# Kernel tuning notes

Measured on AMD Instinct MI355X. Metric: run time of the kernel, lower is better.

The kernel has to match this reference:

```python
import jax, jax.numpy as jnp
import numpy as np

L = 2        # n_layer
D = 1024     # hidden_size
H = 8        # n_head
DK = D // H  # head_dim = 128
DV = D // H
T = 2048     # max_seq_length
B = 4
INTER = 2816 # fla GatedMLP: int(1024*4*2/3)=2730 rounded up to multiple of 256
EPS = 1e-6


def rmsnorm(x, w):
    return x * jax.lax.rsqrt(jnp.mean(x * x, axis=-1, keepdims=True) + EPS) * w


def l2norm(x):
    return x * jax.lax.rsqrt(jnp.sum(x * x, axis=-1, keepdims=True) + EPS)


def delta_attn(x, Wq, Wk, Wv, Wb, Wo, onorm_w):
    # x: [B, T, D]
    b, t, _ = x.shape
    q = jax.nn.silu((x @ Wq).reshape(b, t, H, DK))
    k = jax.nn.silu((x @ Wk).reshape(b, t, H, DK))
    q = l2norm(q)
    k = l2norm(k)
    v = jax.nn.silu((x @ Wv).reshape(b, t, H, DV))
    beta = jax.nn.sigmoid(x @ Wb) * 2.0  # [B,T,H], allow_neg_eigval=True
    # time-major for scan
    qt = q.transpose(1, 0, 2, 3)  # [T,B,H,DK]
    kt = k.transpose(1, 0, 2, 3)
    vt = v.transpose(1, 0, 2, 3)
    bt = beta.transpose(1, 0, 2)  # [T,B,H]

    def step(S, inps):
        qi, ki, vi, bi = inps
        # delta rule: S_t = S_{t-1} + beta_t * k_t (v_t - S_{t-1}^T k_t)^T
        pred = jnp.einsum('bhkv,bhk->bhv', S, ki)
        S = S + bi[..., None, None] * ki[..., :, None] * (vi - pred)[..., None, :]
        o = jnp.einsum('bhkv,bhk->bhv', S, qi)
        return S, o

    S0 = jnp.zeros((b, H, DK, DV), x.dtype)
    _, o = jax.lax.scan(step, S0, (qt, kt, vt, bt))  # o: [T,B,H,DV]
    o = rmsnorm(o, onorm_w)  # per-head RMSNorm (use_gate=False)
    o = o.transpose(1, 0, 2, 3).reshape(b, t, H * DV)
    return o @ Wo


def setup_inputs() -> dict:
    key = jax.random.key(0)
    ks = jax.random.split(key, 13)
    s = 0.02
    f32 = jnp.float32
    return {
        'input_embeds': jax.random.normal(ks[0], (T, B, D), f32),
        'Wq': jax.random.normal(ks[1], (L, D, D), f32) * s,
        'Wk': jax.random.normal(ks[2], (L, D, D), f32) * s,
        'Wv': jax.random.normal(ks[3], (L, D, D), f32) * s,
        'Wb': jax.random.normal(ks[4], (L, D, H), f32) * s,
        'Wo': jax.random.normal(ks[5], (L, D, D), f32) * s,
        'onorm_w': jnp.ones((L, DV), f32) + jax.random.normal(ks[6], (L, DV), f32) * 0.02,
        'norm1_w': jnp.ones((L, D), f32) + jax.random.normal(ks[7], (L, D), f32) * 0.02,
        'norm2_w': jnp.ones((L, D), f32) + jax.random.normal(ks[8], (L, D), f32) * 0.02,
        'Wg': jax.random.normal(ks[9], (L, D, 2 * INTER), f32) * s,
        'Wd': jax.random.normal(ks[10], (L, INTER, D), f32) * s,
        'final_norm_w': jnp.ones((D,), f32) + jax.random.normal(ks[11], (D,), f32) * 0.02,
    }


def reference(input_embeds, Wq, Wk, Wv, Wb, Wo, onorm_w, norm1_w, norm2_w, Wg, Wd, final_norm_w):
    # wrapper transposes (T,B,D) -> (B,T,D)
    x = input_embeds.transpose(1, 0, 2)
    for l in range(L):
        h = rmsnorm(x, norm1_w[l])
        x = x + delta_attn(h, Wq[l], Wk[l], Wv[l], Wb[l], Wo[l], onorm_w[l])
        h = rmsnorm(x, norm2_w[l])
        gy = h @ Wg[l]
        g, y = jnp.split(gy, 2, axis=-1)
        x = x + (jax.nn.silu(g) * y) @ Wd[l]
    x = rmsnorm(x, final_norm_w)
    return x.transpose(1, 0, 2)  # back to (T,B,D)
```

## Files before the change

kernel.cpp:

```cpp
#include <hip/hip_runtime.h>
#include <hip/hip_bf16.h>
#include <cstdint>


typedef _Float16 f16;
typedef __attribute__((ext_vector_type(8))) _Float16 h8;
typedef __attribute__((ext_vector_type(4))) _Float16 h4;
typedef __attribute__((ext_vector_type(4))) float f4;

#define DEV __device__ __forceinline__

static constexpr int Bb_ = 4;
static constexpr int Hh  = 8;
static constexpr int Dd  = 1024;
static constexpr int Tt  = 2048;
static constexpr int NC  = 32;

DEV float siluf(float x) { return x / (1.f + expf(-x)); }

#define AS1(p) ((const __attribute__((address_space(1))) void*)(uintptr_t)(p))
#define AS3(p) ((__attribute__((address_space(3))) void*)(uint32_t)(uintptr_t)(p))

DEV void stage_half(const f16* __restrict__ srcRowBase, int K, int kt,
                    f16* dstHalf, int tid) {
#pragma unroll
  for (int i = 0; i < 2; ++i) {
    const int q = i * 512 + tid;
    const int r = q >> 3, cs = q & 7;
    const int cl = cs ^ (r & 7);
    __builtin_amdgcn_global_load_lds(AS1(srcRowBase + (size_t)r * K + kt * 64 + cl * 8),
                                     AS3(dstHalf + q * 8), 16, 0, 0);
  }
}
DEV h8 rd_sw(const f16* T, int row, int chunk) {
  return *(const h8*)(T + (((row << 3) | (chunk ^ (row & 7))) * 8));
}

template<int EPI, int BN>
__global__ __launch_bounds__(512, 2) void gemm2(const f16* __restrict__ A, const f16* __restrict__ Bt,
                                                void* __restrict__ C, const f16* __restrict__ Yp,
                                                int M, int N, int K, int gx) {
  constexpr int NCF = BN / 64;
  __shared__ __align__(16) f16 ldsA[2][16384];
  __shared__ __align__(16) f16 ldsB[2][BN * 64];
  const int tid = threadIdx.x, lane = tid & 63, w = tid >> 6;
  const int l15 = lane & 15, l4 = lane >> 4;
  const int wr = w >> 2, wc = w & 3;
  const int nwg = gridDim.x;
  int flat = blockIdx.x;
  if ((nwg & 7) == 0) flat = (flat & 7) * (nwg >> 3) + (flat >> 3);
  const int bx = flat % gx, by = flat / gx;

  const f16* Ab = A + (size_t)by * 256 * K;
  const f16* Bb = Bt + (size_t)bx * BN * K;
  const int NT = K >> 6;
  f4 acc[8][NCF] = {};

  stage_half(Bb, K, 0, ldsB[0], tid);
  if (BN == 256) stage_half(Bb + (size_t)128 * K, K, 0, ldsB[0] + 8192, tid);
  stage_half(Ab, K, 0, ldsA[0], tid);
  stage_half(Ab + (size_t)128 * K, K, 0, ldsA[0] + 8192, tid);
  if (NT > 1) {
    stage_half(Bb, K, 1, ldsB[1], tid);
    if (BN == 256) stage_half(Bb + (size_t)128 * K, K, 1, ldsB[1] + 8192, tid);
    if (BN == 256) asm volatile("s_waitcnt vmcnt(4)");
    else           asm volatile("s_waitcnt vmcnt(2)");
  } else {
    asm volatile("s_waitcnt vmcnt(0)");
  }
  __builtin_amdgcn_s_barrier();

  for (int t = 0; t < NT; ++t) {
    const int cur = t & 1, nxt = cur ^ 1;
    const f16* cA = ldsA[cur];
    const f16* cB = ldsB[cur];
    h8 b[NCF][2];
    h8 a[2][2];
#pragma unroll
    for (int cf = 0; cf < NCF; ++cf)
#pragma unroll
      for (int ks = 0; ks < 2; ++ks)
        b[cf][ks] = rd_sw(cB, wc * (BN / 4) + cf * 16 + l15, ks * 4 + l4);
#pragma unroll
    for (int fr = 0; fr < 2; ++fr)
#pragma unroll
      for (int ks = 0; ks < 2; ++ks)
        a[fr][ks] = rd_sw(cA, wr * 128 + fr * 16 + l15, ks * 4 + l4);
    if (t + 1 < NT) stage_half(Ab, K, t + 1, ldsA[nxt], tid);
    __builtin_amdgcn_s_barrier();
    asm volatile("s_waitcnt lgkmcnt(0)");
    __builtin_amdgcn_s_setprio(1);
#pragma unroll
    for (int fr = 0; fr < 2; ++fr)
#pragma unroll
      for (int cf = 0; cf < NCF; ++cf)
#pragma unroll
        for (int ks = 0; ks < 2; ++ks)
          acc[fr][cf] = __builtin_amdgcn_mfma_f32_16x16x32_f16(a[fr][ks], b[cf][ks], acc[fr][cf], 0, 0, 0);
    __builtin_amdgcn_s_setprio(0);
    __builtin_amdgcn_s_barrier();
#pragma unroll
    for (int p = 1; p < 4; ++p) {
#pragma unroll
      for (int fr = 0; fr < 2; ++fr)
#pragma unroll
        for (int ks = 0; ks < 2; ++ks)
          a[fr][ks] = rd_sw(cA, wr * 128 + p * 32 + fr * 16 + l15, ks * 4 + l4);
      if (p == 1 && t + 1 < NT) stage_half(Ab + (size_t)128 * K, K, t + 1, ldsA[nxt] + 8192, tid);
      if (p == 2 && t + 2 < NT) stage_half(Bb, K, t + 2, ldsB[cur], tid);
      if (BN == 256 && p == 3 && t + 2 < NT) stage_half(Bb + (size_t)128 * K, K, t + 2, ldsB[cur] + 8192, tid);
      __builtin_amdgcn_s_barrier();
      asm volatile("s_waitcnt lgkmcnt(0)");
      __builtin_amdgcn_s_setprio(1);
#pragma unroll
      for (int fr = 0; fr < 2; ++fr)
#pragma unroll
        for (int cf = 0; cf < NCF; ++cf)
#pragma unroll
          for (int ks = 0; ks < 2; ++ks)
            acc[p * 2 + fr][cf] = __builtin_amdgcn_mfma_f32_16x16x32_f16(a[fr][ks], b[cf][ks], acc[p * 2 + fr][cf], 0, 0, 0);
      __builtin_amdgcn_s_setprio(0);
      if (p == 3) {
        if (t + 2 < NT) {
          if (BN == 256) asm volatile("s_waitcnt vmcnt(4)");
          else           asm volatile("s_waitcnt vmcnt(2)");
        } else if (t + 1 < NT) {
          asm volatile("s_waitcnt vmcnt(0)");
        }
      }
      __builtin_amdgcn_s_barrier();
    }
  }

#pragma unroll
  for (int fr = 0; fr < 8; ++fr) {
#pragma unroll
    for (int cf = 0; cf < NCF; ++cf) {
      const int row0 = by * 256 + wr * 128 + fr * 16 + l4 * 4;
      const int col = bx * BN + wc * (BN / 4) + cf * 16 + l15;
#pragma unroll
      for (int q = 0; q < 4; ++q) {
        const size_t idx = (size_t)(row0 + q) * N + col;
        const float v = acc[fr][cf][q];
        if (EPI == 0) ((float*)C)[idx] = v;
        if (EPI == 1) ((f16*)C)[idx] = (f16)((float)((f16*)C)[idx] + v);
        if (EPI == 2) ((f16*)C)[idx] = (f16)v;
        if (EPI == 3) ((f16*)C)[idx] = (f16)(siluf(v) * (float)Yp[idx]);
      }
    }
  }
}

__global__ __launch_bounds__(256) void cvt_k(const float* __restrict__ in, f16* __restrict__ out) {
  const size_t i = ((size_t)blockIdx.x * 256 + threadIdx.x) * 8;
  const float4 a = *(const float4*)(in + i);
  const float4 b = *(const float4*)(in + i + 4);
  h8 o = {(f16)a.x, (f16)a.y, (f16)a.z, (f16)a.w, (f16)b.x, (f16)b.y, (f16)b.z, (f16)b.w};
  *(h8*)(out + i) = o;
}

template<int OUT_F16>
__global__ __launch_bounds__(256) void rmsnorm_k(const f16* __restrict__ x, const float* __restrict__ w,
                                                 void* __restrict__ out) {
  const int r = blockIdx.x, tid = threadIdx.x;
  const h4 xv = *(const h4*)(x + (size_t)r * 1024 + tid * 4);
  const float v0 = (float)xv[0], v1 = (float)xv[1], v2 = (float)xv[2], v3 = (float)xv[3];
  float ss = v0 * v0 + v1 * v1 + v2 * v2 + v3 * v3;
#pragma unroll
  for (int m = 1; m < 64; m <<= 1) ss += __shfl_xor(ss, m);
  __shared__ float red[4];
  if ((tid & 63) == 0) red[tid >> 6] = ss;
  __syncthreads();
  const float scale = rsqrtf((red[0] + red[1] + red[2] + red[3]) * (1.f / 1024.f) + 1e-6f);
  const float4 w4 = *(const float4*)(w + tid * 4);
  float o0 = v0 * scale * w4.x, o1 = v1 * scale * w4.y, o2 = v2 * scale * w4.z, o3 = v3 * scale * w4.w;
  if (OUT_F16) {
    h4 o = {(f16)o0, (f16)o1, (f16)o2, (f16)o3};
    *(h4*)((f16*)out + (size_t)r * 1024 + tid * 4) = o;
  } else {
    *(float4*)((float*)out + (size_t)r * 1024 + tid * 4) = make_float4(o0, o1, o2, o3);
  }
}

__global__ __launch_bounds__(256) void qkv_epi(const f16* __restrict__ qkv, f16* __restrict__ qb,
                                               f16* __restrict__ kb, f16* __restrict__ vb) {
  const int r = blockIdx.x, tid = threadIdx.x;
  const int head = tid >> 5, l32 = tid & 31;
  const size_t src = (size_t)r * 3072 + head * 128 + l32 * 4;
  const size_t dst = (size_t)r * 1024 + head * 128 + l32 * 4;
  {
    const h4 v = *(const h4*)(qkv + src);
    float s0 = siluf((float)v[0]), s1 = siluf((float)v[1]), s2 = siluf((float)v[2]), s3 = siluf((float)v[3]);
    float ss = s0 * s0 + s1 * s1 + s2 * s2 + s3 * s3;
#pragma unroll
    for (int m = 1; m <= 16; m <<= 1) ss += __shfl_xor(ss, m);
    const float sc = rsqrtf(ss + 1e-6f);
    h4 o = {(f16)(s0 * sc), (f16)(s1 * sc), (f16)(s2 * sc), (f16)(s3 * sc)};
    *(h4*)(qb + dst) = o;
  }
  {
    const h4 v = *(const h4*)(qkv + src + 1024);
    float s0 = siluf((float)v[0]), s1 = siluf((float)v[1]), s2 = siluf((float)v[2]), s3 = siluf((float)v[3]);
    float ss = s0 * s0 + s1 * s1 + s2 * s2 + s3 * s3;
#pragma unroll
    for (int m = 1; m <= 16; m <<= 1) ss += __shfl_xor(ss, m);
    const float sc = rsqrtf(ss + 1e-6f);
    h4 o = {(f16)(s0 * sc), (f16)(s1 * sc), (f16)(s2 * sc), (f16)(s3 * sc)};
    *(h4*)(kb + dst) = o;
  }
  {
    const h4 v = *(const h4*)(qkv + (size_t)r * 3072 + 2048 + tid * 4);
    h4 o = {(f16)siluf((float)v[0]), (f16)siluf((float)v[1]), (f16)siluf((float)v[2]), (f16)siluf((float)v[3])};
    *(h4*)(vb + (size_t)r * 1024 + tid * 4) = o;
  }
}

__global__ __launch_bounds__(256) void onorm_k(const float* __restrict__ o, const float* __restrict__ w,
                                               f16* __restrict__ ob) {
  const int r = blockIdx.x, tid = threadIdx.x;
  const int head = tid >> 5, l32 = tid & 31;
  const size_t base = (size_t)r * 1024 + head * 128 + l32 * 4;
  const float4 v = *(const float4*)(o + base);
  float ss = v.x * v.x + v.y * v.y + v.z * v.z + v.w * v.w;
#pragma unroll
  for (int m = 1; m <= 16; m <<= 1) ss += __shfl_xor(ss, m);
  const float sc = rsqrtf(ss * (1.f / 128.f) + 1e-6f);
  const float4 w4 = *(const float4*)(w + l32 * 4);
  h4 out = {(f16)(v.x * sc * w4.x), (f16)(v.y * sc * w4.y), (f16)(v.z * sc * w4.z), (f16)(v.w * sc * w4.w)};
  *(h4*)(ob + base) = out;
}

__global__ __launch_bounds__(256) void beta_k(const f16* __restrict__ hb, const float* __restrict__ Wb,
                                              float* __restrict__ beta) {
  const int tid = threadIdx.x, lane = tid & 63, wv = tid >> 6;
  const int r = blockIdx.x * 4 + wv;
  const f16* row = hb + (size_t)r * 1024 + lane * 16;
  const h8 v0 = *(const h8*)(row);
  const h8 v1 = *(const h8*)(row + 8);
  const float* wb = Wb + (size_t)(lane * 16) * 8;
  float acc[8] = {};
#pragma unroll
  for (int e = 0; e < 8; ++e) {
    const float x0 = (float)v0[e], x1 = (float)v1[e];
    const float4 w0a = *(const float4*)(wb + e * 8);
    const float4 w0b = *(const float4*)(wb + e * 8 + 4);
    const float4 w1a = *(const float4*)(wb + (e + 8) * 8);
    const float4 w1b = *(const float4*)(wb + (e + 8) * 8 + 4);
    acc[0] += x0 * w0a.x + x1 * w1a.x;  acc[1] += x0 * w0a.y + x1 * w1a.y;
    acc[2] += x0 * w0a.z + x1 * w1a.z;  acc[3] += x0 * w0a.w + x1 * w1a.w;
    acc[4] += x0 * w0b.x + x1 * w1b.x;  acc[5] += x0 * w0b.y + x1 * w1b.y;
    acc[6] += x0 * w0b.z + x1 * w1b.z;  acc[7] += x0 * w0b.w + x1 * w1b.w;
  }
#pragma unroll
  for (int j = 0; j < 8; ++j)
#pragma unroll
    for (int m = 1; m < 64; m <<= 1) acc[j] += __shfl_xor(acc[j], m);
  if (lane == 0) {
#pragma unroll
    for (int j = 0; j < 8; ++j) beta[(size_t)r * 8 + j] = 2.f / (1.f + expf(-acc[j]));
  }
}

__global__ __launch_bounds__(256) void transpose_k(const float* __restrict__ W, f16* __restrict__ Wt,
                                                   int K, int N) {
  __shared__ float tile[32][33];
  const int n0 = blockIdx.x * 32, k0 = blockIdx.y * 32;
  const int tx = threadIdx.x & 31, ty = threadIdx.x >> 5;
#pragma unroll
  for (int i = 0; i < 32; i += 8) tile[ty + i][tx] = W[(size_t)(k0 + ty + i) * N + n0 + tx];
  __syncthreads();
#pragma unroll
  for (int i = 0; i < 32; i += 8) Wt[(size_t)(n0 + ty + i) * K + k0 + tx] = (f16)tile[tx][ty + i];
}

__global__ void fill_k(float* p, int n, float v) {
  const int i = blockIdx.x * 256 + threadIdx.x;
  if (i < n) p[i] = v;
}

DEV f4 mm16(const f16* A, int as, const f16* B, f4 c, int l15, int l4) {
  h4 a = *(const h4*)(A + l15 * as + l4 * 4);
  h4 b = *(const h4*)(B + l15 * 20 + l4 * 4);
  return __builtin_amdgcn_mfma_f32_16x16x16f16(a, b, c, 0, 0, 0);
}
DEV void wr_T(f16* slot, f4 acc, int l15, int l4, float sgn) {
  h4 v = {(f16)(sgn * acc[0]), (f16)(sgn * acc[1]), (f16)(sgn * acc[2]), (f16)(sgn * acc[3])};
  *(h4*)(slot + l15 * 20 + l4 * 4) = v;
}
DEV void wr_Tb(f16* Tb, int bi, int bj, f4 acc, const float* betas, int l15, int l4, float sgn) {
  const float bc = betas[bj * 16 + l15];
#pragma unroll
  for (int q = 0; q < 4; ++q)
    Tb[(bi * 16 + l4 * 4 + q) * 72 + bj * 16 + l15] = (f16)(sgn * acc[q] * bc);
}

__global__ __launch_bounds__(256) void phaseA(const f16* __restrict__ kb, const f16* __restrict__ qb,
                                              const f16* __restrict__ vb, const float* __restrict__ beta,
                                              f16* __restrict__ wbuf, f16* __restrict__ ubuf,
                                              f16* __restrict__ pbuf) {
  const int blk = blockIdx.x;
  const int c = blk >> 5, bh = blk & 31;
  const int b = bh >> 3, h = bh & 7;
  const int tid = threadIdx.x, lane = tid & 63, wv = tid >> 6;
  const int l15 = lane & 15, l4 = lane >> 4;

  __shared__ __align__(16) f16 Ks[64 * 128];
  __shared__ __align__(16) f16 QVs[64 * 128];
  __shared__ __align__(16) f16 Abuf[64 * 68];
  __shared__ __align__(16) f16 Dr[4][16 * 20];
  __shared__ __align__(16) f16 Dt[4][16 * 20];
  __shared__ __align__(16) f16 Tp[3][16 * 20];
  __shared__ __align__(16) f16 Xp[3][16 * 20];
  __shared__ __align__(16) f16 Tb[64 * 72];
  __shared__ float betas[64];

  const size_t rowstr = (size_t)Bb_ * Dd;
  const size_t gbase = ((size_t)(c * 64) * Bb_ + b) * Dd + h * 128;

#pragma unroll
  for (int i = 0; i < 4; ++i) {
    const int ch = tid + i * 256;
    const int rr = ch >> 4, kc = ch & 15;
    *(h8*)(Ks + ch * 8) = *(const h8*)(kb + gbase + (size_t)rr * rowstr + kc * 8);
    *(h8*)(QVs + ch * 8) = *(const h8*)(qb + gbase + (size_t)rr * rowstr + kc * 8);
  }
  for (int i = tid; i < 64 * 72; i += 256) Tb[i] = (f16)0.f;
  if (tid < 64) betas[tid] = beta[((size_t)(c * 64 + tid) * Bb_ + b) * Hh + h];
  __syncthreads();

  f4 accS[4] = {}, accP[4] = {};
  const int arow = wv * 16 + l15;
  const int koff = l4 * 8;
#pragma unroll
  for (int kc = 0; kc < 4; ++kc) {
    const h8 aK = *(const h8*)(Ks + arow * 128 + kc * 32 + koff);
    const h8 aQ = *(const h8*)(QVs + arow * 128 + kc * 32 + koff);
#pragma unroll
    for (int f = 0; f < 4; ++f) {
      const h8 bK = *(const h8*)(Ks + (f * 16 + l15) * 128 + kc * 32 + koff);
      accS[f] = __builtin_amdgcn_mfma_f32_16x16x32_f16(aK, bK, accS[f], 0, 0, 0);
      accP[f] = __builtin_amdgcn_mfma_f32_16x16x32_f16(aQ, bK, accP[f], 0, 0, 0);
    }
  }
  const size_t pbase = (((size_t)bh * NC + c) * 64) * 64;
#pragma unroll
  for (int f = 0; f < 4; ++f) {
#pragma unroll
    for (int q = 0; q < 4; ++q) {
      const int i = wv * 16 + l4 * 4 + q;
      const int j = f * 16 + l15;
      Abuf[i * 68 + j] = (f16)((j < i) ? betas[i] * accS[f][q] : 0.f);
      pbuf[pbase + (size_t)i * 64 + j] = (f16)((j <= i) ? accP[f][q] : 0.f);
    }
  }
  __syncthreads();

#pragma unroll
  for (int i = 0; i < 4; ++i) {
    const int ch = tid + i * 256;
    const int rr = ch >> 4, kc = ch & 15;
    *(h8*)(QVs + ch * 8) = *(const h8*)(vb + gbase + (size_t)rr * rowstr + kc * 8);
  }

  {
    const int bi = wv;
    const int cc = l15;
    const f16* Ad = Abuf + (bi * 16) * 68 + bi * 16;
    float t[16];
    t[0] = (cc == 0) ? 1.f : 0.f;
#pragma unroll
    for (int i = 1; i < 16; ++i) {
      float s = (cc == i) ? 1.f : 0.f;
#pragma unroll
      for (int j = 0; j < i; ++j) s -= (float)Ad[i * 68 + j] * t[j];
      t[i] = s;
    }
    if (lane < 16) {
#pragma unroll
      for (int j4 = 0; j4 < 4; ++j4) {
        h4 v = {(f16)t[j4 * 4], (f16)t[j4 * 4 + 1], (f16)t[j4 * 4 + 2], (f16)t[j4 * 4 + 3]};
        *(h4*)(&Dt[bi][cc * 20 + j4 * 4]) = v;
      }
      const float bc = betas[bi * 16 + cc];
#pragma unroll
      for (int j = 0; j < 16; ++j) {
        Dr[bi][j * 20 + cc] = (f16)t[j];
        Tb[(bi * 16 + j) * 72 + bi * 16 + cc] = (f16)(t[j] * bc);
      }
    }
  }
  __syncthreads();

  const f16* AB10 = Abuf + 16 * 68 + 0;
  const f16* AB20 = Abuf + 32 * 68 + 0;
  const f16* AB21 = Abuf + 32 * 68 + 16;
  const f16* AB30 = Abuf + 48 * 68 + 0;
  const f16* AB31 = Abuf + 48 * 68 + 16;
  const f16* AB32 = Abuf + 48 * 68 + 32;
  f4 z = {};
  f4 x20, x30;

  if (wv == 0) wr_T(Xp[0], mm16(AB10, 68, Dt[0], z, l15, l4), l15, l4, 1.f);
  if (wv == 1) wr_T(Xp[1], mm16(AB21, 68, Dt[1], z, l15, l4), l15, l4, 1.f);
  if (wv == 2) wr_T(Xp[2], mm16(AB32, 68, Dt[2], z, l15, l4), l15, l4, 1.f);
  if (wv == 3) x20 = mm16(AB20, 68, Dt[0], z, l15, l4);
  __syncthreads();
  if (wv == 0) { f4 r = mm16(Dr[1], 20, Xp[0], z, l15, l4); wr_T(Tp[0], r, l15, l4, -1.f); wr_Tb(Tb, 1, 0, r, betas, l15, l4, -1.f); }
  if (wv == 1) { f4 r = mm16(Dr[2], 20, Xp[1], z, l15, l4); wr_T(Tp[1], r, l15, l4, -1.f); wr_Tb(Tb, 2, 1, r, betas, l15, l4, -1.f); }
  if (wv == 2) { f4 r = mm16(Dr[3], 20, Xp[2], z, l15, l4); wr_Tb(Tb, 3, 2, r, betas, l15, l4, -1.f); }
  if (wv == 3) x30 = mm16(AB30, 68, Dt[0], z, l15, l4);
  __syncthreads();
  if (wv == 3) wr_T(Xp[0], mm16(AB21, 68, Tp[0], x20, l15, l4), l15, l4, 1.f);
  if (wv == 1) { f4 r = mm16(AB31, 68, Dt[1], z, l15, l4); r = mm16(AB32, 68, Tp[1], r, l15, l4); wr_T(Xp[1], r, l15, l4, 1.f); }
  __syncthreads();
  if (wv == 3) { f4 r = mm16(Dr[2], 20, Xp[0], z, l15, l4); wr_T(Tp[2], r, l15, l4, -1.f); wr_Tb(Tb, 2, 0, r, betas, l15, l4, -1.f); }
  if (wv == 1) { f4 r = mm16(Dr[3], 20, Xp[1], z, l15, l4); wr_Tb(Tb, 3, 1, r, betas, l15, l4, -1.f); }
  __syncthreads();
  if (wv == 3) { f4 r = mm16(AB31, 68, Tp[0], x30, l15, l4); r = mm16(AB32, 68, Tp[2], r, l15, l4); wr_T(Xp[2], r, l15, l4, 1.f); }
  __syncthreads();
  if (wv == 3) { f4 r = mm16(Dr[3], 20, Xp[2], z, l15, l4); wr_Tb(Tb, 3, 0, r, betas, l15, l4, -1.f); }
  __syncthreads();

  const size_t wub = ((size_t)bh * Tt + c * 64) * 128;
  f4 wacc[8] = {}, uacc[8] = {};
#pragma unroll
  for (int kc = 0; kc < 2; ++kc) {
    const h8 aT = *(const h8*)(Tb + (wv * 16 + l15) * 72 + kc * 32 + koff);
#pragma unroll
    for (int f = 0; f < 8; ++f) {
      h8 bK, bV;
#pragma unroll
      for (int j = 0; j < 8; ++j) {
        const int t2 = kc * 32 + koff + j;
        const int d = f * 16 + l15;
        bK[j] = Ks[t2 * 128 + d];
        bV[j] = QVs[t2 * 128 + d];
      }
      wacc[f] = __builtin_amdgcn_mfma_f32_16x16x32_f16(aT, bK, wacc[f], 0, 0, 0);
      uacc[f] = __builtin_amdgcn_mfma_f32_16x16x32_f16(aT, bV, uacc[f], 0, 0, 0);
    }
  }
#pragma unroll
  for (int f = 0; f < 8; ++f)
#pragma unroll
    for (int q = 0; q < 4; ++q) {
      const int i = wv * 16 + l4 * 4 + q;
      const int d = f * 16 + l15;
      wbuf[wub + (size_t)i * 128 + d] = (f16)wacc[f][q];
      ubuf[wub + (size_t)i * 128 + d] = (f16)uacc[f][q];
    }
}

__global__ __launch_bounds__(256) void phaseB(const f16* __restrict__ qb, const f16* __restrict__ kb,
                                              const f16* __restrict__ wbuf, const f16* __restrict__ ubuf,
                                              const f16* __restrict__ pbuf, float* __restrict__ obuf) {
  const int blk = blockIdx.x;
  const int bh = blk >> 2, g = blk & 3;
  const int b = bh >> 3, h = bh & 7;
  const int tid = threadIdx.x, lane = tid & 63, wv = tid >> 6;
  const int l15 = lane & 15, l4 = lane >> 4;

  __shared__ __align__(16) f16 Ws[64 * 128];
  __shared__ __align__(16) f16 Qs[64 * 128];
  __shared__ __align__(16) f16 Ks[64 * 128];
  __shared__ __align__(16) f16 Ps[64 * 64];
  __shared__ __align__(16) f16 Rt[32 * 72];
  __shared__ __align__(16) f16 Ms[32 * 136];

  for (int i = tid; i < 32 * 136; i += 256) Ms[i] = (f16)0.f;
  f4 macc[2][2] = {};

  const size_t rowstr = (size_t)Bb_ * Dd;
  const size_t qk0 = (size_t)b * Dd + h * 128;
  const int arow = wv * 16 + l15;
  const int koff = l4 * 8;
  __syncthreads();

  for (int c = 0; c < NC; ++c) {
    const size_t wub = ((size_t)bh * Tt + c * 64) * 128;
    const size_t pbase = (((size_t)bh * NC + c) * 64) * 64;
#pragma unroll
    for (int i = 0; i < 4; ++i) {
      const int ch = tid + i * 256;
      const int rr = ch >> 4, kc = ch & 15;
      *(h8*)(Ws + ch * 8) = *(const h8*)(wbuf + wub + ch * 8);
      *(h8*)(Qs + ch * 8) = *(const h8*)(qb + qk0 + (size_t)(c * 64 + rr) * rowstr + kc * 8);
      *(h8*)(Ks + ch * 8) = *(const h8*)(kb + qk0 + (size_t)(c * 64 + rr) * rowstr + kc * 8);
    }
#pragma unroll
    for (int i = 0; i < 2; ++i) {
      const int ch = tid + i * 256;
      *(h8*)(Ps + ch * 8) = *(const h8*)(pbuf + pbase + ch * 8);
    }
    __syncthreads();

    f4 accR[2] = {}, accO[2] = {};
#pragma unroll
    for (int kc = 0; kc < 4; ++kc) {
      const h8 aW = *(const h8*)(Ws + arow * 128 + kc * 32 + koff);
      const h8 aQ = *(const h8*)(Qs + arow * 128 + kc * 32 + koff);
#pragma unroll
      for (int f = 0; f < 2; ++f) {
        const h8 bM = *(const h8*)(Ms + (f * 16 + l15) * 136 + kc * 32 + koff);
        accR[f] = __builtin_amdgcn_mfma_f32_16x16x32_f16(aW, bM, accR[f], 0, 0, 0);
        accO[f] = __builtin_amdgcn_mfma_f32_16x16x32_f16(aQ, bM, accO[f], 0, 0, 0);
      }
    }
#pragma unroll
    for (int f = 0; f < 2; ++f) {
#pragma unroll
      for (int q = 0; q < 4; ++q) {
        const int i = wv * 16 + l4 * 4 + q;
        const int cc = f * 16 + l15;
        const float uv = (float)ubuf[wub + (size_t)i * 128 + g * 32 + cc];
        const float rv = uv - accR[f][q];
        accR[f][q] = rv;
        Rt[cc * 72 + i] = (f16)rv;
      }
    }
    __syncthreads();

#pragma unroll
    for (int kc = 0; kc < 2; ++kc) {
      const h8 aP = *(const h8*)(Ps + arow * 64 + kc * 32 + koff);
#pragma unroll
      for (int f = 0; f < 2; ++f) {
        const h8 bR = *(const h8*)(Rt + (f * 16 + l15) * 72 + kc * 32 + koff);
        accO[f] = __builtin_amdgcn_mfma_f32_16x16x32_f16(aP, bR, accO[f], 0, 0, 0);
      }
    }
#pragma unroll
    for (int f = 0; f < 2; ++f)
#pragma unroll
      for (int q = 0; q < 4; ++q) {
        const int i = wv * 16 + l4 * 4 + q;
        const int cc = f * 16 + l15;
        obuf[((size_t)(c * 64 + i) * Bb_ + b) * Dd + h * 128 + g * 32 + cc] = accO[f][q];
      }

#pragma unroll
    for (int kc = 0; kc < 2; ++kc) {
      const h8 aR0 = *(const h8*)(Rt + l15 * 72 + kc * 32 + koff);
      const h8 aR1 = *(const h8*)(Rt + (16 + l15) * 72 + kc * 32 + koff);
#pragma unroll
      for (int cf = 0; cf < 2; ++cf) {
        const int kcol = wv * 32 + cf * 16 + l15;
        h8 bKv;
#pragma unroll
        for (int j = 0; j < 8; ++j) bKv[j] = Ks[(kc * 32 + koff + j) * 128 + kcol];
        macc[0][cf] = __builtin_amdgcn_mfma_f32_16x16x32_f16(aR0, bKv, macc[0][cf], 0, 0, 0);
        macc[1][cf] = __builtin_amdgcn_mfma_f32_16x16x32_f16(aR1, bKv, macc[1][cf], 0, 0, 0);
      }
    }
#pragma unroll
    for (int rf = 0; rf < 2; ++rf)
#pragma unroll
      for (int cf = 0; cf < 2; ++cf)
#pragma unroll
        for (int q = 0; q < 4; ++q) {
          const int cr = rf * 16 + l4 * 4 + q;
          const int kcol = wv * 32 + cf * 16 + l15;
          Ms[cr * 136 + kcol] = (f16)macc[rf][cf][q];
        }
    __syncthreads();
  }
}

extern "C" void kernel_launch(void* const* d_in, const int* in_sizes, int n_in,
                              void* d_out, int out_size, void* d_ws, size_t ws_size,
                              hipStream_t stream) {
  (void)in_sizes; (void)n_in;
  const float* input = (const float*)d_in[0];
  const float* Wq = (const float*)d_in[1];
  const float* Wk = (const float*)d_in[2];
  const float* Wv = (const float*)d_in[3];
  const float* Wb = (const float*)d_in[4];
  const float* Wo = (const float*)d_in[5];
  const float* onw = (const float*)d_in[6];
  const float* n1w = (const float*)d_in[7];
  const float* n2w = (const float*)d_in[8];
  const float* Wg = (const float*)d_in[9];
  const float* Wd = (const float*)d_in[10];
  const float* fnw = (const float*)d_in[11];

  char* ws = (char*)d_ws;
  size_t off = 0;
  auto alloc = [&](size_t bytes) { void* p = ws + off; off += (bytes + 255) & ~(size_t)255; return p; };
  const size_t RD = 8192ull * 1024ull;
  f16*  x     = (f16*)alloc(RD * 2);
  f16*  hb    = (f16*)alloc(RD * 2);
  f16*  qb    = (f16*)alloc(RD * 2);
  f16*  kbuf  = (f16*)alloc(RD * 2);
  f16*  vbuf  = (f16*)alloc(RD * 2);
  float* beta = (float*)alloc(8192ull * 8 * 4);
  f16*  wbuf  = (f16*)alloc(RD * 2);
  f16*  ubuf  = (f16*)alloc(RD * 2);
  f16*  pbuf  = (f16*)alloc(32ull * 32 * 64 * 64 * 2);
  char* arena = (char*)alloc(3 * RD * 2);
  f16*  WqkvT = (f16*)alloc(3072ull * 1024 * 2);
  f16*  WoT   = (f16*)alloc(1024ull * 1024 * 2);
  f16*  WgT   = (f16*)alloc(5632ull * 1024 * 2);
  f16*  WdT   = (f16*)alloc(1024ull * 2816 * 2);
  if (off > ws_size) {
    fill_k<<<(out_size + 255) / 256, 256, 0, stream>>>((float*)d_out, out_size, 1.0e6f);
    return;
  }
  f16* qkvraw = (f16*)arena;
  float* obuf = (float*)arena;
  f16* Ybuf = (f16*)arena;
  f16* my = qb;
  f16* ob = wbuf;

  cvt_k<<<4096, 256, 0, stream>>>(input, x);

  for (int l = 0; l < 2; ++l) {
    const size_t o2 = (size_t)l * 1024 * 1024;
    transpose_k<<<dim3(32, 32), 256, 0, stream>>>(Wq + o2, WqkvT, 1024, 1024);
    transpose_k<<<dim3(32, 32), 256, 0, stream>>>(Wk + o2, WqkvT + 1024ull * 1024, 1024, 1024);
    transpose_k<<<dim3(32, 32), 256, 0, stream>>>(Wv + o2, WqkvT + 2048ull * 1024, 1024, 1024);
    transpose_k<<<dim3(32, 32), 256, 0, stream>>>(Wo + o2, WoT, 1024, 1024);
    transpose_k<<<dim3(176, 32), 256, 0, stream>>>(Wg + (size_t)l * 1024 * 5632, WgT, 1024, 5632);
    transpose_k<<<dim3(32, 88), 256, 0, stream>>>(Wd + (size_t)l * 2816 * 1024, WdT, 2816, 1024);

    rmsnorm_k<1><<<8192, 256, 0, stream>>>(x, n1w + l * 1024, hb);
    gemm2<2, 256><<<32 * 12, 512, 0, stream>>>(hb, WqkvT, qkvraw, nullptr, 8192, 3072, 1024, 12);
    beta_k<<<2048, 256, 0, stream>>>(hb, Wb + (size_t)l * 1024 * 8, beta);
    qkv_epi<<<8192, 256, 0, stream>>>(qkvraw, qb, kbuf, vbuf);
    phaseA<<<1024, 256, 0, stream>>>(kbuf, qb, vbuf, beta, wbuf, ubuf, pbuf);
    phaseB<<<128, 256, 0, stream>>>(qb, kbuf, wbuf, ubuf, pbuf, obuf);
    onorm_k<<<8192, 256, 0, stream>>>(obuf, onw + l * 128, ob);
    gemm2<1, 128><<<32 * 8, 512, 0, stream>>>(ob, WoT, x, nullptr, 8192, 1024, 1024, 8);

    rmsnorm_k<1><<<8192, 256, 0, stream>>>(x, n2w + l * 1024, hb);
    gemm2<2, 256><<<32 * 11, 512, 0, stream>>>(hb, WgT + 2816ull * 1024, Ybuf, nullptr, 8192, 2816, 1024, 11);
    gemm2<3, 256><<<32 * 11, 512, 0, stream>>>(hb, WgT, my, Ybuf, 8192, 2816, 1024, 11);
    gemm2<1, 128><<<32 * 8, 512, 0, stream>>>(my, WdT, x, nullptr, 8192, 1024, 2816, 8);
  }
  rmsnorm_k<0><<<8192, 256, 0, stream>>>(x, fnw, d_out);
}
```

Baseline: 1.142 ms.

## Double-buffer phaseB chunk loads, pre-transpose K/U, swizzle q/k/v layouts

New measurement: 1.064 ms. 6.8% less time.

```diff
diff --git a/kernel.cpp b/kernel.cpp
--- a/kernel.cpp
+++ b/kernel.cpp
@@ -17,6 +17,7 @@
 static constexpr int NC  = 32;
 
 DEV float siluf(float x) { return x / (1.f + expf(-x)); }
+DEV int swz16(int row, int c) { return (c & 8) | ((c & 7) ^ (row & 7)); }
 
 #define AS1(p) ((const __attribute__((address_space(1))) void*)(uintptr_t)(p))
 #define AS3(p) ((__attribute__((address_space(3))) void*)(uint32_t)(uintptr_t)(p))
@@ -186,8 +187,8 @@
                                                f16* __restrict__ kb, f16* __restrict__ vb) {
   const int r = blockIdx.x, tid = threadIdx.x;
   const int head = tid >> 5, l32 = tid & 31;
+  const int i = (r >> 2) & 63;
   const size_t src = (size_t)r * 3072 + head * 128 + l32 * 4;
-  const size_t dst = (size_t)r * 1024 + head * 128 + l32 * 4;
   {
     const h4 v = *(const h4*)(qkv + src);
     float s0 = siluf((float)v[0]), s1 = siluf((float)v[1]), s2 = siluf((float)v[2]), s3 = siluf((float)v[3]);
@@ -196,7 +197,8 @@
     for (int m = 1; m <= 16; m <<= 1) ss += __shfl_xor(ss, m);
     const float sc = rsqrtf(ss + 1e-6f);
     h4 o = {(f16)(s0 * sc), (f16)(s1 * sc), (f16)(s2 * sc), (f16)(s3 * sc)};
-    *(h4*)(qb + dst) = o;
+    const int c = l32 >> 1, off = (l32 & 1) * 4;
+    *(h4*)(qb + (size_t)r * 1024 + head * 128 + swz16(i, c) * 8 + off) = o;
   }
   {
     const h4 v = *(const h4*)(qkv + src + 1024);
@@ -206,27 +208,31 @@
     for (int m = 1; m <= 16; m <<= 1) ss += __shfl_xor(ss, m);
     const float sc = rsqrtf(ss + 1e-6f);
     h4 o = {(f16)(s0 * sc), (f16)(s1 * sc), (f16)(s2 * sc), (f16)(s3 * sc)};
-    *(h4*)(kb + dst) = o;
+    const int c = l32 >> 1, off = (l32 & 1) * 4;
+    *(h4*)(kb + (size_t)r * 1024 + head * 128 + swz16(i, c) * 8 + off) = o;
   }
   {
     const h4 v = *(const h4*)(qkv + (size_t)r * 3072 + 2048 + tid * 4);
     h4 o = {(f16)siluf((float)v[0]), (f16)siluf((float)v[1]), (f16)siluf((float)v[2]), (f16)siluf((float)v[3])};
-    *(h4*)(vb + (size_t)r * 1024 + tid * 4) = o;
-  }
-}
-
-__global__ __launch_bounds__(256) void onorm_k(const float* __restrict__ o, const float* __restrict__ w,
+    const int hd = tid >> 5, dh = (tid & 31) * 4;
+    const int c = dh >> 3, off = dh & 7;
+    *(h4*)(vb + (size_t)r * 1024 + hd * 128 + swz16(i, c) * 8 + off) = o;
+  }
+}
+
+__global__ __launch_bounds__(256) void onorm_k(const f16* __restrict__ o, const float* __restrict__ w,
                                                f16* __restrict__ ob) {
   const int r = blockIdx.x, tid = threadIdx.x;
   const int head = tid >> 5, l32 = tid & 31;
   const size_t base = (size_t)r * 1024 + head * 128 + l32 * 4;
-  const float4 v = *(const float4*)(o + base);
-  float ss = v.x * v.x + v.y * v.y + v.z * v.z + v.w * v.w;
+  const h4 xv = *(const h4*)(o + base);
+  const float v0 = (float)xv[0], v1 = (float)xv[1], v2 = (float)xv[2], v3 = (float)xv[3];
+  float ss = v0 * v0 + v1 * v1 + v2 * v2 + v3 * v3;
 #pragma unroll
   for (int m = 1; m <= 16; m <<= 1) ss += __shfl_xor(ss, m);
   const float sc = rsqrtf(ss * (1.f / 128.f) + 1e-6f);
   const float4 w4 = *(const float4*)(w + l32 * 4);
-  h4 out = {(f16)(v.x * sc * w4.x), (f16)(v.y * sc * w4.y), (f16)(v.z * sc * w4.z), (f16)(v.w * sc * w4.w)};
+  h4 out = {(f16)(v0 * sc * w4.x), (f16)(v1 * sc * w4.y), (f16)(v2 * sc * w4.z), (f16)(v3 * sc * w4.w)};
   *(h4*)(ob + base) = out;
 }
 
@@ -296,8 +302,8 @@
 
 __global__ __launch_bounds__(256) void phaseA(const f16* __restrict__ kb, const f16* __restrict__ qb,
                                               const f16* __restrict__ vb, const float* __restrict__ beta,
-                                              f16* __restrict__ wbuf, f16* __restrict__ ubuf,
-                                              f16* __restrict__ pbuf) {
+                                              f16* __restrict__ wbuf, f16* __restrict__ utbuf,
+                                              f16* __restrict__ pbuf, f16* __restrict__ ktbuf) {
   const int blk = blockIdx.x;
   const int c = blk >> 5, bh = blk & 31;
   const int b = bh >> 3, h = bh & 7;
@@ -330,14 +336,15 @@
 
   f4 accS[4] = {}, accP[4] = {};
   const int arow = wv * 16 + l15;
-  const int koff = l4 * 8;
 #pragma unroll
   for (int kc = 0; kc < 4; ++kc) {
-    const h8 aK = *(const h8*)(Ks + arow * 128 + kc * 32 + koff);
-    const h8 aQ = *(const h8*)(QVs + arow * 128 + kc * 32 + koff);
+    const int c4 = kc * 4 + l4;
+    const h8 aK = *(const h8*)(Ks + arow * 128 + swz16(arow, c4) * 8);
+    const h8 aQ = *(const h8*)(QVs + arow * 128 + swz16(arow, c4) * 8);
 #pragma unroll
     for (int f = 0; f < 4; ++f) {
-      const h8 bK = *(const h8*)(Ks + (f * 16 + l15) * 128 + kc * 32 + koff);
+      const int brow = f * 16 + l15;
+      const h8 bK = *(const h8*)(Ks + brow * 128 + swz16(brow, c4) * 8);
       accS[f] = __builtin_amdgcn_mfma_f32_16x16x32_f16(aK, bK, accS[f], 0, 0, 0);
       accP[f] = __builtin_amdgcn_mfma_f32_16x16x32_f16(aQ, bK, accP[f], 0, 0, 0);
     }
@@ -421,84 +428,111 @@
   if (wv == 3) { f4 r = mm16(Dr[3], 20, Xp[2], z, l15, l4); wr_Tb(Tb, 3, 0, r, betas, l15, l4, -1.f); }
   __syncthreads();
 
-  const size_t wub = ((size_t)bh * Tt + c * 64) * 128;
+  const size_t wub = ((size_t)bh * NC + c) * 8192;
+  const int koff = l4 * 8;
   f4 wacc[8] = {}, uacc[8] = {};
 #pragma unroll
   for (int kc = 0; kc < 2; ++kc) {
     const h8 aT = *(const h8*)(Tb + (wv * 16 + l15) * 72 + kc * 32 + koff);
 #pragma unroll
     for (int f = 0; f < 8; ++f) {
+      const int d = f * 16 + l15, cD = d >> 3, d7 = d & 7;
       h8 bK, bV;
 #pragma unroll
       for (int j = 0; j < 8; ++j) {
         const int t2 = kc * 32 + koff + j;
-        const int d = f * 16 + l15;
-        bK[j] = Ks[t2 * 128 + d];
-        bV[j] = QVs[t2 * 128 + d];
+        const int pos = t2 * 128 + swz16(t2, cD) * 8 + d7;
+        bK[j] = Ks[pos];
+        bV[j] = QVs[pos];
       }
       wacc[f] = __builtin_amdgcn_mfma_f32_16x16x32_f16(aT, bK, wacc[f], 0, 0, 0);
       uacc[f] = __builtin_amdgcn_mfma_f32_16x16x32_f16(aT, bV, uacc[f], 0, 0, 0);
     }
   }
 #pragma unroll
-  for (int f = 0; f < 8; ++f)
+  for (int f = 0; f < 8; ++f) {
+    const int d = f * 16 + l15, cD = d >> 3, d7 = d & 7;
 #pragma unroll
     for (int q = 0; q < 4; ++q) {
       const int i = wv * 16 + l4 * 4 + q;
-      const int d = f * 16 + l15;
-      wbuf[wub + (size_t)i * 128 + d] = (f16)wacc[f][q];
-      ubuf[wub + (size_t)i * 128 + d] = (f16)uacc[f][q];
-    }
-}
-
-__global__ __launch_bounds__(256) void phaseB(const f16* __restrict__ qb, const f16* __restrict__ kb,
-                                              const f16* __restrict__ wbuf, const f16* __restrict__ ubuf,
-                                              const f16* __restrict__ pbuf, float* __restrict__ obuf) {
+      wbuf[wub + (size_t)i * 128 + swz16(i, cD) * 8 + d7] = (f16)wacc[f][q];
+    }
+    h4 uv = {(f16)uacc[f][0], (f16)uacc[f][1], (f16)uacc[f][2], (f16)uacc[f][3]};
+    *(h4*)(utbuf + wub + (size_t)d * 64 + wv * 16 + l4 * 4) = uv;
+  }
+
+#pragma unroll
+  for (int i2 = 0; i2 < 4; ++i2) {
+    const int ch = tid + i2 * 256;
+    const int dp = ch & 127, c2 = ch >> 7;
+    h8 v;
+#pragma unroll
+    for (int j = 0; j < 8; ++j) {
+      const int i = c2 * 8 + j;
+      v[j] = Ks[i * 128 + swz16(i, dp >> 3) * 8 + (dp & 7)];
+    }
+    *(h8*)(ktbuf + wub + (size_t)dp * 64 + (c2 ^ (dp & 7)) * 8) = v;
+  }
+}
+
+__global__ __launch_bounds__(256) void phaseB(const f16* __restrict__ qb, const f16* __restrict__ ktbuf,
+                                              const f16* __restrict__ wbuf, const f16* __restrict__ utbuf,
+                                              const f16* __restrict__ pbuf, f16* __restrict__ obuf) {
   const int blk = blockIdx.x;
   const int bh = blk >> 2, g = blk & 3;
   const int b = bh >> 3, h = bh & 7;
   const int tid = threadIdx.x, lane = tid & 63, wv = tid >> 6;
   const int l15 = lane & 15, l4 = lane >> 4;
 
-  __shared__ __align__(16) f16 Ws[64 * 128];
-  __shared__ __align__(16) f16 Qs[64 * 128];
-  __shared__ __align__(16) f16 Ks[64 * 128];
-  __shared__ __align__(16) f16 Ps[64 * 64];
+  __shared__ __align__(16) f16 Ws[2][8192];
+  __shared__ __align__(16) f16 Qs[2][8192];
+  __shared__ __align__(16) f16 Kts[2][8192];
   __shared__ __align__(16) f16 Rt[32 * 72];
   __shared__ __align__(16) f16 Ms[32 * 136];
 
   for (int i = tid; i < 32 * 136; i += 256) Ms[i] = (f16)0.f;
   f4 macc[2][2] = {};
 
-  const size_t rowstr = (size_t)Bb_ * Dd;
-  const size_t qk0 = (size_t)b * Dd + h * 128;
   const int arow = wv * 16 + l15;
   const int koff = l4 * 8;
-  __syncthreads();
-
-  for (int c = 0; c < NC; ++c) {
-    const size_t wub = ((size_t)bh * Tt + c * 64) * 128;
-    const size_t pbase = (((size_t)bh * NC + c) * 64) * 64;
+
+  auto STAGE = [&](int c2, int buf) {
 #pragma unroll
     for (int i = 0; i < 4; ++i) {
       const int ch = tid + i * 256;
-      const int rr = ch >> 4, kc = ch & 15;
-      *(h8*)(Ws + ch * 8) = *(const h8*)(wbuf + wub + ch * 8);
-      *(h8*)(Qs + ch * 8) = *(const h8*)(qb + qk0 + (size_t)(c * 64 + rr) * rowstr + kc * 8);
-      *(h8*)(Ks + ch * 8) = *(const h8*)(kb + qk0 + (size_t)(c * 64 + rr) * rowstr + kc * 8);
-    }
-#pragma unroll
-    for (int i = 0; i < 2; ++i) {
-      const int ch = tid + i * 256;
-      *(h8*)(Ps + ch * 8) = *(const h8*)(pbuf + pbase + ch * 8);
-    }
-    __syncthreads();
+      const size_t tb = ((size_t)bh * NC + c2) * 8192;
+      __builtin_amdgcn_global_load_lds(AS1(wbuf + tb + ch * 8), AS3(Ws[buf] + ch * 8), 16, 0, 0);
+      __builtin_amdgcn_global_load_lds(AS1(ktbuf + tb + ch * 8), AS3(Kts[buf] + ch * 8), 16, 0, 0);
+      const int rr = ch >> 4, kc2 = ch & 15;
+      __builtin_amdgcn_global_load_lds(AS1(qb + ((size_t)((c2 * 64 + rr) * 4 + b)) * 1024 + h * 128 + kc2 * 8),
+                                       AS3(Qs[buf] + ch * 8), 16, 0, 0);
+    }
+  };
+
+  STAGE(0, 0);
+  asm volatile("s_waitcnt vmcnt(0)" ::: "memory");
+  __builtin_amdgcn_s_barrier();
+
+  for (int c = 0; c < NC; ++c) {
+    const int cur = c & 1, nxt = cur ^ 1;
+    const size_t pcb = ((size_t)bh * NC + c) * 4096;
+    const h8 aP0 = *(const h8*)(pbuf + pcb + arow * 64 + koff);
+    const h8 aP1 = *(const h8*)(pbuf + pcb + arow * 64 + 32 + koff);
+    const size_t ucb = ((size_t)bh * NC + c) * 8192;
+    const h4 u0 = *(const h4*)(utbuf + ucb + (size_t)(g * 32 + l15) * 64 + wv * 16 + l4 * 4);
+    const h4 u1 = *(const h4*)(utbuf + ucb + (size_t)(g * 32 + 16 + l15) * 64 + wv * 16 + l4 * 4);
+    asm volatile("s_waitcnt vmcnt(4)" ::: "memory");
+    asm volatile("s_waitcnt lgkmcnt(0)" ::: "memory");
+    __builtin_amdgcn_s_barrier();
+    if (c + 1 < NC) STAGE(c + 1, nxt);
 
     f4 accR[2] = {}, accO[2] = {};
+    __builtin_amdgcn_s_setprio(1);
 #pragma unroll
     for (int kc = 0; kc < 4; ++kc) {
-      const h8 aW = *(const h8*)(Ws + arow * 128 + kc * 32 + koff);
-      const h8 aQ = *(const h8*)(Qs + arow * 128 + kc * 32 + koff);
+      const int c4 = kc * 4 + l4;
+      const h8 aW = *(const h8*)(Ws[cur] + arow * 128 + swz16(arow, c4) * 8);
+      const h8 aQ = *(const h8*)(Qs[cur] + arow * 128 + swz16(arow, c4) * 8);
 #pragma unroll
       for (int f = 0; f < 2; ++f) {
         const h8 bM = *(const h8*)(Ms + (f * 16 + l15) * 136 + kc * 32 + koff);
@@ -506,36 +540,40 @@
         accO[f] = __builtin_amdgcn_mfma_f32_16x16x32_f16(aQ, bM, accO[f], 0, 0, 0);
       }
     }
+    __builtin_amdgcn_s_setprio(0);
+    if (c + 1 < NC) asm volatile("s_waitcnt vmcnt(12)" ::: "memory");
+    else            asm volatile("s_waitcnt vmcnt(0)" ::: "memory");
 #pragma unroll
     for (int f = 0; f < 2; ++f) {
+      const h4 uu = f ? u1 : u0;
+      h4 rw;
+#pragma unroll
+      for (int q = 0; q < 4; ++q) {
+        const float rv = (float)uu[q] - accR[f][q];
+        accR[f][q] = rv;
+        rw[q] = (f16)rv;
+      }
+      *(h4*)(Rt + (f * 16 + l15) * 72 + wv * 16 + l4 * 4) = rw;
+    }
+    asm volatile("s_waitcnt lgkmcnt(0)" ::: "memory");
+    __builtin_amdgcn_s_barrier();
+
+#pragma unroll
+    for (int kc = 0; kc < 2; ++kc) {
+      const h8 aP = kc ? aP1 : aP0;
+#pragma unroll
+      for (int f = 0; f < 2; ++f) {
+        const h8 bR = *(const h8*)(Rt + (f * 16 + l15) * 72 + kc * 32 + koff);
+        accO[f] = __builtin_amdgcn_mfma_f32_16x16x32_f16(aP, bR, accO[f], 0, 0, 0);
+      }
+    }
+#pragma unroll
+    for (int f = 0; f < 2; ++f)
 #pragma unroll
       for (int q = 0; q < 4; ++q) {
         const int i = wv * 16 + l4 * 4 + q;
         const int cc = f * 16 + l15;
-        const float uv = (float)ubuf[wub + (size_t)i * 128 + g * 32 + cc];
-        const float rv = uv - accR[f][q];
-        accR[f][q] = rv;
-        Rt[cc * 72 + i] = (f16)rv;
-      }
-    }
-    __syncthreads();
-
-#pragma unroll
-    for (int kc = 0; kc < 2; ++kc) {
-      const h8 aP = *(const h8*)(Ps + arow * 64 + kc * 32 + koff);
-#pragma unroll
-      for (int f = 0; f < 2; ++f) {
-        const h8 bR = *(const h8*)(Rt + (f * 16 + l15) * 72 + kc * 32 + koff);
-        accO[f] = __builtin_amdgcn_mfma_f32_16x16x32_f16(aP, bR, accO[f], 0, 0, 0);
-      }
-    }
-#pragma unroll
-    for (int f = 0; f < 2; ++f)
-#pragma unroll
-      for (int q = 0; q < 4; ++q) {
-        const int i = wv * 16 + l4 * 4 + q;
-        const int cc = f * 16 + l15;
-        obuf[((size_t)(c * 64 + i) * Bb_ + b) * Dd + h * 128 + g * 32 + cc] = accO[f][q];
+        obuf[((size_t)(c * 64 + i) * Bb_ + b) * Dd + h * 128 + g * 32 + cc] = (f16)accO[f][q];
       }
 
 #pragma unroll
@@ -545,9 +583,8 @@
 #pragma unroll
       for (int cf = 0; cf < 2; ++cf) {
         const int kcol = wv * 32 + cf * 16 + l15;
-        h8 bKv;
-#pragma unroll
-        for (int j = 0; j < 8; ++j) bKv[j] = Ks[(kc * 32 + koff + j) * 128 + kcol];
+        const int c2 = kc * 4 + l4;
+        const h8 bKv = *(const h8*)(Kts[cur] + kcol * 64 + (c2 ^ (kcol & 7)) * 8);
         macc[0][cf] = __builtin_amdgcn_mfma_f32_16x16x32_f16(aR0, bKv, macc[0][cf], 0, 0, 0);
         macc[1][cf] = __builtin_amdgcn_mfma_f32_16x16x32_f16(aR1, bKv, macc[1][cf], 0, 0, 0);
       }
@@ -562,7 +599,6 @@
           const int kcol = wv * 32 + cf * 16 + l15;
           Ms[cr * 136 + kcol] = (f16)macc[rf][cf][q];
         }
-    __syncthreads();
   }
 }
 
@@ -594,7 +630,8 @@
   f16*  vbuf  = (f16*)alloc(RD * 2);
   float* beta = (float*)alloc(8192ull * 8 * 4);
   f16*  wbuf  = (f16*)alloc(RD * 2);
-  f16*  ubuf  = (f16*)alloc(RD * 2);
+  f16*  utbuf = (f16*)alloc(RD * 2);
+  f16*  ktbuf = (f16*)alloc(RD * 2);
   f16*  pbuf  = (f16*)alloc(32ull * 32 * 64 * 64 * 2);
   char* arena = (char*)alloc(3 * RD * 2);
   f16*  WqkvT = (f16*)alloc(3072ull * 1024 * 2);
@@ -606,7 +643,7 @@
     return;
   }
   f16* qkvraw = (f16*)arena;
-  float* obuf = (float*)arena;
+  f16* obuf = (f16*)arena;
   f16* Ybuf = (f16*)arena;
   f16* my = qb;
   f16* ob = wbuf;
@@ -626,8 +663,8 @@
     gemm2<2, 256><<<32 * 12, 512, 0, stream>>>(hb, WqkvT, qkvraw, nullptr, 8192, 3072, 1024, 12);
     beta_k<<<2048, 256, 0, stream>>>(hb, Wb + (size_t)l * 1024 * 8, beta);
     qkv_epi<<<8192, 256, 0, stream>>>(qkvraw, qb, kbuf, vbuf);
-    phaseA<<<1024, 256, 0, stream>>>(kbuf, qb, vbuf, beta, wbuf, ubuf, pbuf);
-    phaseB<<<128, 256, 0, stream>>>(qb, kbuf, wbuf, ubuf, pbuf, obuf);
+    phaseA<<<1024, 256, 0, stream>>>(kbuf, qb, vbuf, beta, wbuf, utbuf, pbuf, ktbuf);
+    phaseB<<<128, 256, 0, stream>>>(qb, ktbuf, wbuf, utbuf, pbuf, obuf);
     onorm_k<<<8192, 256, 0, stream>>>(obuf, onw + l * 128, ob);
     gemm2<1, 128><<<32 * 8, 512, 0, stream>>>(ob, WoT, x, nullptr, 8192, 1024, 1024, 8);
 
```
